# Kernel tuning notes

Measured on AMD Instinct MI355X. Metric: run time of the kernel, lower is better.

The kernel has to match this reference:

```python
import jax, jax.numpy as jnp
import numpy as np

B, C, H, W = 8, 256, 128, 128
INTER = 64      # in_channels // 4
C8 = INTER // 8 # query/key channels


def setup_inputs() -> dict:
    key = jax.random.key(0)
    ks = jax.random.split(key, 12)
    f = lambda k, shp, s=0.05: (jax.random.normal(k, shp, jnp.float32) * s)
    return dict(
        x_exmplar=f(ks[0], (B, C, H, W), 1.0),
        x_query=f(ks[1], (B, C, H, W), 1.0),
        conv_ex_w=f(ks[2], (INTER, C, 3, 3)),
        bn_ex_s=jnp.ones((INTER,), jnp.float32), bn_ex_b=jnp.zeros((INTER,), jnp.float32),
        conv_q_w=f(ks[3], (INTER, C, 3, 3)),
        bn_q_s=jnp.ones((INTER,), jnp.float32), bn_q_b=jnp.zeros((INTER,), jnp.float32),
        q_w=f(ks[4], (C8, INTER)), q_b=jnp.zeros((C8,), jnp.float32),
        k_w=f(ks[5], (C8, INTER)), k_b=jnp.zeros((C8,), jnp.float32),
        v_w=f(ks[6], (INTER, INTER)), v_b=jnp.zeros((INTER,), jnp.float32),
        gamma_1=jnp.float32(0.1), gamma_2=jnp.float32(0.1),
        tail_ex_w=f(ks[7], (C, INTER, 3, 3)),
        bn_tex_s=jnp.ones((C,), jnp.float32), bn_tex_b=jnp.zeros((C,), jnp.float32),
        tail_q_w=f(ks[8], (C, INTER, 3, 3)),
        bn_tq_s=jnp.ones((C,), jnp.float32), bn_tq_b=jnp.zeros((C,), jnp.float32),
    )


def _conv_bn_relu(x, w, s, b):
    # 3x3 conv (pad 1, no bias) + eval-mode BatchNorm (running mean 0 / var 1 at init) + ReLU
    y = jax.lax.conv_general_dilated(x, w, (1, 1), ((1, 1), (1, 1)),
                                     dimension_numbers=('NCHW', 'OIHW', 'NCHW'))
    return jax.nn.relu(y * s[None, :, None, None] + b[None, :, None, None])


def _rattention(xe, xq, qw, qb, kw, kb, vw, vb, g1, g2):
    b_, c_, h_, w_ = xq.shape
    q = jnp.einsum('oc,bchw->bohw', qw, xq) + qb[None, :, None, None]  # [B,C8,H,W]
    k = jnp.einsum('oc,bchw->bohw', kw, xe) + kb[None, :, None, None]
    v = jnp.einsum('oc,bchw->bohw', vw, xe) + vb[None, :, None, None]  # [B,INTER,H,W]
    # column (H-axis) energies, diagonal (self) masked with -inf
    eH = jnp.einsum('bciw,bcjw->biwj', q, k)                    # [B,H,W,H]
    diag = jnp.eye(h_, dtype=bool)[None, :, None, :]            # (1,H,1,H) over (i,j)
    eH = jnp.where(diag, -jnp.inf, eH)
    # row (W-axis) energies (no mask, matches original)
    eW = jnp.einsum('bchi,bchj->bhij', q, k)                    # [B,H,W,W]
    att = jax.nn.softmax(jnp.concatenate([eH, eW], axis=-1), axis=-1)
    attH, attW = att[..., :h_], att[..., h_:]
    outH = jnp.einsum('bcjw,bhwj->bchw', v, attH)
    outW = jnp.einsum('bchj,bhwj->bchw', v, attW)
    # LR diagonal branch; softmax over trailing singleton dim == ones (kept for fidelity)
    qd = jnp.diagonal(q, axis1=2, axis2=3)                      # [B,C8,H]
    kd = jnp.diagonal(k, axis1=2, axis2=3).transpose(0, 2, 1)   # [B,H,C8]
    vd = jnp.diagonal(v, axis1=2, axis2=3)                      # [B,INTER,H]
    eLR = jnp.einsum('bhc,bcj->bhj', kd, qd)                    # [B,H,H]
    outLR = jax.nn.softmax(jnp.einsum('bch,bhj->bcj', vd, eLR)[..., None], axis=3)  # [B,INTER,H,1]
    # RL branch: diagonal of the transposed map == same main diagonal -> identical to LR
    outRL = outLR
    s = outH + outW + outLR + outRL   # broadcast (B,INTER,H,1) over W
    return g1 * s + xe, g2 * s + xq


def reference(x_exmplar, x_query, conv_ex_w, bn_ex_s, bn_ex_b, conv_q_w, bn_q_s, bn_q_b,
              q_w, q_b, k_w, k_b, v_w, v_b, gamma_1, gamma_2,
              tail_ex_w, bn_tex_s, bn_tex_b, tail_q_w, bn_tq_s, bn_tq_b):
    xe = _conv_bn_relu(x_exmplar, conv_ex_w, bn_ex_s, bn_ex_b)
    xq = _conv_bn_relu(x_query, conv_q_w, bn_q_s, bn_q_b)
    for _ in range(2):  # recurrence=2
        xe, xq = _rattention(xe, xq, q_w, q_b, k_w, k_b, v_w, v_b, gamma_1, gamma_2)
    xe = _conv_bn_relu(xe, tail_ex_w, bn_tex_s, bn_tex_b)
    xq = _conv_bn_relu(xq, tail_q_w, bn_tq_s, bn_tq_b)
    return xe, xq
```

## Files before the change

### kernel.cpp

```cpp
#include <hip/hip_runtime.h>

constexpr int BB = 8;
constexpr int CC = 256;
constexpr int HH = 128;
constexpr int WW = 128;
constexpr int INTER = 64;
constexpr size_t NPIX = (size_t)HH * WW;
constexpr size_t C64SZ = (size_t)BB * INTER * NPIX;
constexpr size_t QSZ   = (size_t)BB * 8 * NPIX;
constexpr size_t STATSZ = (size_t)BB * HH * WW;
constexpr size_t OUTHALF = (size_t)BB * CC * NPIX;
constexpr size_t WT_ELEMS = (size_t)9 * 64 * 256;

typedef __attribute__((ext_vector_type(8))) __bf16 bf16x8;
typedef __attribute__((ext_vector_type(4))) float f32x4;
typedef __attribute__((ext_vector_type(4))) short short4v;

__device__ inline short f2bf(float f) {
    union { float f; unsigned u; } a; a.f = f;
    unsigned r = a.u + 0x7fffu + ((a.u >> 16) & 1u);
    return (short)(r >> 16);
}

__global__ __launch_bounds__(256) void wprep_kernel(
    const float* __restrict__ wgt, short* __restrict__ wt, int OC, int IC)
{
    int idx = blockIdx.x * 256 + threadIdx.x;
    int n = 9 * OC * IC;
    if (idx >= n) return;
    int ic = idx & (IC - 1);
    int t  = idx / IC;
    int oc = t & (OC - 1);
    int pos = t / OC;
    wt[idx] = f2bf(wgt[((size_t)oc * IC + ic) * 9 + pos]);
}

template<int IC, int OC, int R, int NT>
__global__ __launch_bounds__(256, 2) void conv_mfma(
    const float* __restrict__ x, const short* __restrict__ wt,
    const float* __restrict__ bns, const float* __restrict__ bnb,
    float* __restrict__ out)
{
    constexpr int ROWS = R + 2;
    constexpr int NCH  = IC / 32;
    constexpr int NPIXT = R * 128;
    constexpr int NWN  = NPIXT / (NT * 16);

    __shared__ __align__(16) short xs[ROWS * 130 * 40];

    const int tid = threadIdx.x;
    const int b   = blockIdx.x;
    const int h0  = blockIdx.y * R;
    const int l   = tid & 63;
    const int ln  = l & 15;
    const int q   = l >> 4;
    const int wv  = tid >> 6;
    const int nbase = (wv % NWN) * (NT * 16);
    const int oc0w  = (wv / NWN) * 64;

    f32x4 acc[4][NT];
#pragma unroll
    for (int mt = 0; mt < 4; ++mt)
#pragma unroll
        for (int nt = 0; nt < NT; ++nt)
            acc[mt][nt] = (f32x4){0.f, 0.f, 0.f, 0.f};

    const float* xb = x + (size_t)b * IC * NPIX;

    for (int ch = 0; ch < NCH; ++ch) {
        const int ic0 = ch * 32;
        constexpr int UNITS = ROWS * 8;
        for (int u = 0; u < UNITS; u += 2) {
            int unit = u + (tid >> 7);
            int col  = tid & 127;
            int row  = unit >> 3;
            int icg  = unit & 7;
            int ic   = ic0 + icg * 4;
            int grow = h0 - 1 + row;
            short4v pk;
            if ((unsigned)grow < 128u) {
                const float* p = xb + ((size_t)ic * 128 + grow) * 128 + col;
                pk.x = f2bf(p[0]);
                pk.y = f2bf(p[16384]);
                pk.z = f2bf(p[32768]);
                pk.w = f2bf(p[49152]);
            } else {
                pk.x = 0; pk.y = 0; pk.z = 0; pk.w = 0;
            }
            *(short4v*)&xs[(row * 130 + col + 1) * 40 + icg * 4] = pk;
        }
        if (tid < ROWS * 16) {
            int row  = tid >> 4;
            int colh = (tid & 8) ? 129 : 0;
            int icg  = tid & 7;
            short4v z; z.x = 0; z.y = 0; z.z = 0; z.w = 0;
            *(short4v*)&xs[(row * 130 + colh) * 40 + icg * 4] = z;
        }
        __syncthreads();

        for (int dh = 0; dh < 3; ++dh) {
#pragma unroll
            for (int dw = 0; dw < 3; ++dw) {
                const int pos = dh * 3 + dw;
                bf16x8 a[4];
#pragma unroll
                for (int mt = 0; mt < 4; ++mt)
                    a[mt] = *(const bf16x8*)(wt +
                        (size_t)(pos * OC + oc0w + mt * 16 + ln) * IC + ic0 + q * 8);
#pragma unroll
                for (int nt = 0; nt < NT; ++nt) {
                    int pix  = nbase + nt * 16 + ln;
                    int rowi = (pix >> 7) + dh;
                    int wpos = (pix & 127) + dw;
                    bf16x8 bfr = *(const bf16x8*)&xs[(rowi * 130 + wpos) * 40 + q * 8];
#pragma unroll
                    for (int mt = 0; mt < 4; ++mt)
                        acc[mt][nt] = __builtin_amdgcn_mfma_f32_16x16x32_bf16(
                            a[mt], bfr, acc[mt][nt], 0, 0, 0);
                }
            }
        }
        __syncthreads();
    }

#pragma unroll
    for (int mt = 0; mt < 4; ++mt) {
#pragma unroll
        for (int r = 0; r < 4; ++r) {
            int oc = oc0w + mt * 16 + q * 4 + r;
            float s   = bns[oc];
            float bb2 = bnb[oc];
#pragma unroll
            for (int nt = 0; nt < NT; ++nt) {
                int pix = nbase + nt * 16 + ln;
                int h = h0 + (pix >> 7), w = pix & 127;
                float v = fmaxf(acc[mt][nt][r] * s + bb2, 0.f);
                out[(((size_t)b * OC + oc) * 128 + h) * 128 + w] = v;
            }
        }
    }
}

__global__ __launch_bounds__(256) void qk_kernel(
    const float* __restrict__ xq, const float* __restrict__ xe,
    const float* __restrict__ qw, const float* __restrict__ qb,
    const float* __restrict__ kw, const float* __restrict__ kb,
    float* __restrict__ q, float* __restrict__ k)
{
    size_t p = (size_t)blockIdx.x * 256 + threadIdx.x;
    int b = (int)(p >> 14);
    int pix = (int)(p & 16383);
    const float* xqb = xq + (size_t)b * 64 * NPIX + pix;
    const float* xeb = xe + (size_t)b * 64 * NPIX + pix;
    float qa[8], ka[8];
#pragma unroll
    for (int o = 0; o < 8; ++o) { qa[o] = qb[o]; ka[o] = kb[o]; }
    for (int c = 0; c < 64; ++c) {
        float xv = xqb[(size_t)c * NPIX];
        float ev = xeb[(size_t)c * NPIX];
#pragma unroll
        for (int o = 0; o < 8; ++o) {
            qa[o] += qw[o * 64 + c] * xv;
            ka[o] += kw[o * 64 + c] * ev;
        }
    }
#pragma unroll
    for (int o = 0; o < 8; ++o) {
        q[((size_t)b * 8 + o) * NPIX + pix] = qa[o];
        k[((size_t)b * 8 + o) * NPIX + pix] = ka[o];
    }
}

__global__ __launch_bounds__(256) void v_kernel(
    const float* __restrict__ xe,
    const float* __restrict__ vw, const float* __restrict__ vb,
    float* __restrict__ v)
{
    size_t p = (size_t)blockIdx.x * 256 + threadIdx.x;
    int b = (int)(p >> 14);
    int pix = (int)(p & 16383);
    int oc0 = blockIdx.y * 32;
    const float* xeb = xe + (size_t)b * 64 * NPIX + pix;
    float acc[32];
#pragma unroll
    for (int o = 0; o < 32; ++o) acc[o] = vb[oc0 + o];
    for (int c = 0; c < 64; ++c) {
        float ev = xeb[(size_t)c * NPIX];
#pragma unroll
        for (int o = 0; o < 32; ++o) acc[o] += vw[(oc0 + o) * 64 + c] * ev;
    }
#pragma unroll
    for (int o = 0; o < 32; ++o)
        v[((size_t)b * 64 + oc0 + o) * NPIX + pix] = acc[o];
}

__global__ __launch_bounds__(256) void attn_col_kernel(
    const float* __restrict__ q, const float* __restrict__ k,
    const float* __restrict__ v,
    float* __restrict__ outT, float* __restrict__ mC, float* __restrict__ sC)
{
    __shared__ float qs[8][128];
    __shared__ float ks[8][128];
    __shared__ float vs[64][129];
    __shared__ float E[32][129];

    const int tid = threadIdx.x;
    const int w = blockIdx.x;
    const int b = blockIdx.y;

    for (int i = tid; i < 1024; i += 256) {
        int c = i >> 7, h = i & 127;
        qs[c][h] = q[(((size_t)b * 8 + c) * 128 + h) * 128 + w];
        ks[c][h] = k[(((size_t)b * 8 + c) * 128 + h) * 128 + w];
    }
    for (int i = tid; i < 8192; i += 256) {
        int c = i >> 7, j = i & 127;
        vs[c][j] = v[(((size_t)b * 64 + c) * 128 + j) * 128 + w];
    }
    __syncthreads();

    const int jj = tid & 127;
    const int hi = tid >> 7;

    for (int hc = 0; hc < 4; ++hc) {
        const int h0 = hc * 32;
#pragma unroll
        for (int e = 0; e < 16; ++e) {
            int i = e * 2 + hi;
            float a = 0.f;
#pragma unroll
            for (int c = 0; c < 8; ++c) a += qs[c][h0 + i] * ks[c][jj];
            if (h0 + i == jj) a = -1e30f;
            E[i][jj] = a;
        }
        __syncthreads();
        if (tid < 32) {
            int i = tid;
            float m = -1e30f;
            for (int j = 0; j < 128; ++j) m = fmaxf(m, E[i][j]);
            float s = 0.f;
            for (int j = 0; j < 128; ++j) {
                float pp = __expf(E[i][j] - m);
                E[i][j] = pp;
                s += pp;
            }
            mC[((size_t)b * 128 + (h0 + i)) * 128 + w] = m;
            sC[((size_t)b * 128 + (h0 + i)) * 128 + w] = s;
        }
        __syncthreads();
        {
            int c0 = (tid & 15) * 4;
            int i0 = (tid >> 4) * 2;
            float acc[4][2];
#pragma unroll
            for (int a = 0; a < 4; ++a) { acc[a][0] = 0.f; acc[a][1] = 0.f; }
            for (int j = 0; j < 128; ++j) {
                float p0 = E[i0][j], p1 = E[i0 + 1][j];
#pragma unroll
                for (int a = 0; a < 4; ++a) {
                    float vv = vs[c0 + a][j];
                    acc[a][0] += vv * p0;
                    acc[a][1] += vv * p1;
                }
            }
#pragma unroll
            for (int a = 0; a < 4; ++a) {
                size_t base = (((size_t)b * 128 + w) * 64 + (c0 + a)) * 128 + h0 + i0;
                outT[base]     = acc[a][0];
                outT[base + 1] = acc[a][1];
            }
        }
        __syncthreads();
    }
}

__global__ __launch_bounds__(256) void attn_row_kernel(
    const float* __restrict__ q, const float* __restrict__ k,
    const float* __restrict__ v,
    float* __restrict__ outS, float* __restrict__ mR, float* __restrict__ sR)
{
    __shared__ float qs[8][128];
    __shared__ float ks[8][128];
    __shared__ float vs[64][129];
    __shared__ float E[32][129];

    const int tid = threadIdx.x;
    const int h = blockIdx.x;
    const int b = blockIdx.y;

    for (int i = tid; i < 1024; i += 256) {
        int c = i >> 7, x = i & 127;
        qs[c][x] = q[(((size_t)b * 8 + c) * 128 + h) * 128 + x];
        ks[c][x] = k[(((size_t)b * 8 + c) * 128 + h) * 128 + x];
    }
    for (int i = tid; i < 8192; i += 256) {
        int c = i >> 7, j = i & 127;
        vs[c][j] = v[(((size_t)b * 64 + c) * 128 + h) * 128 + j];
    }
    __syncthreads();

    const int jj = tid & 127;
    const int hi = tid >> 7;

    for (int wc = 0; wc < 4; ++wc) {
        const int w0 = wc * 32;
#pragma unroll
        for (int e = 0; e < 16; ++e) {
            int i = e * 2 + hi;
            float a = 0.f;
#pragma unroll
            for (int c = 0; c < 8; ++c) a += qs[c][w0 + i] * ks[c][jj];
            E[i][jj] = a;
        }
        __syncthreads();
        if (tid < 32) {
            int i = tid;
            float m = -1e30f;
            for (int j = 0; j < 128; ++j) m = fmaxf(m, E[i][j]);
            float s = 0.f;
            for (int j = 0; j < 128; ++j) {
                float pp = __expf(E[i][j] - m);
                E[i][j] = pp;
                s += pp;
            }
            mR[((size_t)b * 128 + h) * 128 + (w0 + i)] = m;
            sR[((size_t)b * 128 + h) * 128 + (w0 + i)] = s;
        }
        __syncthreads();
        {
            int c0 = (tid & 15) * 4;
            int i0 = (tid >> 4) * 2;
            float acc[4][2];
#pragma unroll
            for (int a = 0; a < 4; ++a) { acc[a][0] = 0.f; acc[a][1] = 0.f; }
            for (int j = 0; j < 128; ++j) {
                float p0 = E[i0][j], p1 = E[i0 + 1][j];
#pragma unroll
                for (int a = 0; a < 4; ++a) {
                    float vv = vs[c0 + a][j];
                    acc[a][0] += vv * p0;
                    acc[a][1] += vv * p1;
                }
            }
#pragma unroll
            for (int a = 0; a < 4; ++a) {
                size_t base = (((size_t)b * 64 + (c0 + a)) * 128 + h) * 128 + w0 + i0;
                outS[base]     = acc[a][0];
                outS[base + 1] = acc[a][1];
            }
        }
        __syncthreads();
    }
}

__global__ __launch_bounds__(256) void merge_kernel(
    const float* __restrict__ T1, const float* __restrict__ S2,
    const float* __restrict__ mC, const float* __restrict__ sC,
    const float* __restrict__ mR, const float* __restrict__ sR,
    const float* __restrict__ g1p, const float* __restrict__ g2p,
    float* __restrict__ xe, float* __restrict__ xq)
{
    __shared__ float mc[128], sc[128], mr[128], sr[128];
    const int tid = threadIdx.x;
    const int h = blockIdx.x;
    const int b = blockIdx.y;
    if (tid < 128) {
        size_t o = ((size_t)b * 128 + h) * 128 + tid;
        mc[tid] = mC[o]; sc[tid] = sC[o];
        mr[tid] = mR[o]; sr[tid] = sR[o];
    }
    float g1 = g1p[0], g2 = g2p[0];
    __syncthreads();
    for (int i = tid; i < 8192; i += 256) {
        int c = i >> 7, w = i & 127;
        float oc_ = T1[(((size_t)b * 128 + w) * 64 + c) * 128 + h];
        float ow_ = S2[(((size_t)b * 64 + c) * 128 + h) * 128 + w];
        float m  = fmaxf(mc[w], mr[w]);
        float ec = __expf(mc[w] - m);
        float er = __expf(mr[w] - m);
        float denom = sc[w] * ec + sr[w] * er;
        float sval = (oc_ * ec + ow_ * er) / denom + 2.0f;
        size_t p = (((size_t)b * 64 + c) * 128 + h) * 128 + w;
        xe[p] += g1 * sval;
        xq[p] += g2 * sval;
    }
}

extern "C" void kernel_launch(void* const* d_in, const int* in_sizes, int n_in,
                              void* d_out, int out_size, void* d_ws, size_t ws_size,
                              hipStream_t stream)
{
    const float* x_ex = (const float*)d_in[0];
    const float* x_q  = (const float*)d_in[1];
    const float* cew  = (const float*)d_in[2];
    const float* bes  = (const float*)d_in[3];
    const float* beb  = (const float*)d_in[4];
    const float* cqw  = (const float*)d_in[5];
    const float* bqs  = (const float*)d_in[6];
    const float* bqb  = (const float*)d_in[7];
    const float* qw   = (const float*)d_in[8];
    const float* qb   = (const float*)d_in[9];
    const float* kw   = (const float*)d_in[10];
    const float* kb   = (const float*)d_in[11];
    const float* vw   = (const float*)d_in[12];
    const float* vb   = (const float*)d_in[13];
    const float* g1   = (const float*)d_in[14];
    const float* g2   = (const float*)d_in[15];
    const float* tew  = (const float*)d_in[16];
    const float* bts  = (const float*)d_in[17];
    const float* btb  = (const float*)d_in[18];
    const float* tqw  = (const float*)d_in[19];
    const float* btqs = (const float*)d_in[20];
    const float* btqb = (const float*)d_in[21];

    float* out = (float*)d_out;

    short* wt0 = (short*)d_ws;
    short* wt1 = wt0 + WT_ELEMS;
    short* wt2 = wt1 + WT_ELEMS;
    short* wt3 = wt2 + WT_ELEMS;
    float* Wf  = (float*)(wt3 + WT_ELEMS);
    float* xe = Wf;
    float* xq = Wf + C64SZ;
    float* v  = Wf + 2 * C64SZ;
    float* q  = Wf + 3 * C64SZ;
    float* k  = q + QSZ;

    float* T1 = out;
    float* S2 = out + C64SZ;
    float* mC = out + 2 * C64SZ;
    float* sC = mC + STATSZ;
    float* mR = sC + STATSZ;
    float* sR = mR + STATSZ;

    wprep_kernel<<<576, 256, 0, stream>>>(cew, wt0, 64, 256);
    wprep_kernel<<<576, 256, 0, stream>>>(cqw, wt1, 64, 256);
    wprep_kernel<<<576, 256, 0, stream>>>(tew, wt2, 256, 64);
    wprep_kernel<<<576, 256, 0, stream>>>(tqw, wt3, 256, 64);

    conv_mfma<256, 64, 2, 4><<<dim3(8, 64), 256, 0, stream>>>(x_ex, wt0, bes, beb, xe);
    conv_mfma<256, 64, 2, 4><<<dim3(8, 64), 256, 0, stream>>>(x_q,  wt1, bqs, bqb, xq);

    for (int round = 0; round < 2; ++round) {
        qk_kernel<<<512, 256, 0, stream>>>(xq, xe, qw, qb, kw, kb, q, k);
        v_kernel<<<dim3(512, 2), 256, 0, stream>>>(xe, vw, vb, v);
        attn_col_kernel<<<dim3(128, 8), 256, 0, stream>>>(q, k, v, T1, mC, sC);
        attn_row_kernel<<<dim3(128, 8), 256, 0, stream>>>(q, k, v, S2, mR, sR);
        merge_kernel<<<dim3(128, 8), 256, 0, stream>>>(T1, S2, mC, sC, mR, sR, g1, g2, xe, xq);
    }

    conv_mfma<64, 256, 1, 8><<<dim3(8, 128), 256, 0, stream>>>(xe, wt2, bts, btb, out);
    conv_mfma<64, 256, 1, 8><<<dim3(8, 128), 256, 0, stream>>>(xq, wt3, btqs, btqb, out + OUTHALF);
}
```

Before: 1.567 ms.

## Prefetch conv input tiles in registers, widen head conv blocks, parallelize softmax

The conv kernel now loads the next 32-channel input chunk into registers with vectorized float4 loads while MFMAs run on the current chunk, then converts and writes it to LDS after a barrier. This is meant to hide global load latency that was previously fully exposed. The head conv moves to 512-thread blocks with fewer N tiles per wave. In both attention kernels the row softmax is spread across all 256 threads with shuffle reductions instead of 32 serial threads. The register prefetch buffer raises register pressure, which may limit occupancy.

Measured after the change: 1.597 ms. About the same (+1.9%).

```diff
diff --git a/kernel.cpp b/kernel.cpp
--- a/kernel.cpp
+++ b/kernel.cpp
@@ -35,8 +35,8 @@
     wt[idx] = f2bf(wgt[((size_t)oc * IC + ic) * 9 + pos]);
 }
 
-template<int IC, int OC, int R, int NT>
-__global__ __launch_bounds__(256, 2) void conv_mfma(
+template<int IC, int OC, int R, int NT, int BLK, int MINW>
+__global__ __launch_bounds__(BLK, MINW) void conv_mfma(
     const float* __restrict__ x, const short* __restrict__ wt,
     const float* __restrict__ bns, const float* __restrict__ bnb,
     float* __restrict__ out)
@@ -45,6 +45,8 @@
     constexpr int NCH  = IC / 32;
     constexpr int NPIXT = R * 128;
     constexpr int NWN  = NPIXT / (NT * 16);
+    constexpr int TOTAL_UNITS = ROWS * 8 * 32;
+    constexpr int NU   = TOTAL_UNITS / BLK;
 
     __shared__ __align__(16) short xs[ROWS * 130 * 40];
 
@@ -67,37 +69,65 @@
 
     const float* xb = x + (size_t)b * IC * NPIX;
 
+    f32x4 pf[NU][4];
+
+    if (tid < ROWS * 16) {
+        int row  = tid >> 4;
+        int colh = (tid & 8) ? 129 : 0;
+        int icg  = tid & 7;
+        short4v z; z.x = 0; z.y = 0; z.z = 0; z.w = 0;
+        *(short4v*)&xs[(row * 130 + colh) * 40 + icg * 4] = z;
+    }
+
+    auto issue = [&](int ch) {
+        const int ic0 = ch * 32;
+#pragma unroll
+        for (int i = 0; i < NU; ++i) {
+            int u    = i * BLK + tid;
+            int row  = u >> 8;
+            int icq  = (u >> 5) & 7;
+            int colq = u & 31;
+            int grow = h0 - 1 + row;
+            if ((unsigned)grow < 128u) {
+                const float* p = xb + ((size_t)(ic0 + icq * 4) * 128 + grow) * 128 + colq * 4;
+#pragma unroll
+                for (int j = 0; j < 4; ++j)
+                    pf[i][j] = *(const f32x4*)(p + (size_t)j * NPIX);
+            } else {
+#pragma unroll
+                for (int j = 0; j < 4; ++j)
+                    pf[i][j] = (f32x4){0.f, 0.f, 0.f, 0.f};
+            }
+        }
+    };
+
+    auto commit = [&]() {
+#pragma unroll
+        for (int i = 0; i < NU; ++i) {
+            int u    = i * BLK + tid;
+            int row  = u >> 8;
+            int icq  = (u >> 5) & 7;
+            int colq = u & 31;
+#pragma unroll
+            for (int k = 0; k < 4; ++k) {
+                short4v pk;
+                pk.x = f2bf(pf[i][0][k]);
+                pk.y = f2bf(pf[i][1][k]);
+                pk.z = f2bf(pf[i][2][k]);
+                pk.w = f2bf(pf[i][3][k]);
+                *(short4v*)&xs[(row * 130 + colq * 4 + k + 1) * 40 + icq * 4] = pk;
+            }
+        }
+    };
+
+    issue(0);
+    commit();
+    __syncthreads();
+
     for (int ch = 0; ch < NCH; ++ch) {
+        if (ch + 1 < NCH) issue(ch + 1);
+
         const int ic0 = ch * 32;
-        constexpr int UNITS = ROWS * 8;
-        for (int u = 0; u < UNITS; u += 2) {
-            int unit = u + (tid >> 7);
-            int col  = tid & 127;
-            int row  = unit >> 3;
-            int icg  = unit & 7;
-            int ic   = ic0 + icg * 4;
-            int grow = h0 - 1 + row;
-            short4v pk;
-            if ((unsigned)grow < 128u) {
-                const float* p = xb + ((size_t)ic * 128 + grow) * 128 + col;
-                pk.x = f2bf(p[0]);
-                pk.y = f2bf(p[16384]);
-                pk.z = f2bf(p[32768]);
-                pk.w = f2bf(p[49152]);
-            } else {
-                pk.x = 0; pk.y = 0; pk.z = 0; pk.w = 0;
-            }
-            *(short4v*)&xs[(row * 130 + col + 1) * 40 + icg * 4] = pk;
-        }
-        if (tid < ROWS * 16) {
-            int row  = tid >> 4;
-            int colh = (tid & 8) ? 129 : 0;
-            int icg  = tid & 7;
-            short4v z; z.x = 0; z.y = 0; z.z = 0; z.w = 0;
-            *(short4v*)&xs[(row * 130 + colh) * 40 + icg * 4] = z;
-        }
-        __syncthreads();
-
         for (int dh = 0; dh < 3; ++dh) {
 #pragma unroll
             for (int dw = 0; dw < 3; ++dw) {
@@ -121,6 +151,10 @@
             }
         }
         __syncthreads();
+        if (ch + 1 < NCH) {
+            commit();
+            __syncthreads();
+        }
     }
 
 #pragma unroll
@@ -234,18 +268,29 @@
             E[i][jj] = a;
         }
         __syncthreads();
-        if (tid < 32) {
-            int i = tid;
+        {
+            int row = tid >> 3, l8 = tid & 7;
             float m = -1e30f;
-            for (int j = 0; j < 128; ++j) m = fmaxf(m, E[i][j]);
+#pragma unroll
+            for (int t = 0; t < 16; ++t) m = fmaxf(m, E[row][l8 + t * 8]);
+            m = fmaxf(m, __shfl_xor(m, 1));
+            m = fmaxf(m, __shfl_xor(m, 2));
+            m = fmaxf(m, __shfl_xor(m, 4));
             float s = 0.f;
-            for (int j = 0; j < 128; ++j) {
-                float pp = __expf(E[i][j] - m);
-                E[i][j] = pp;
+#pragma unroll
+            for (int t = 0; t < 16; ++t) {
+                int j = l8 + t * 8;
+                float pp = __expf(E[row][j] - m);
+                E[row][j] = pp;
                 s += pp;
             }
-            mC[((size_t)b * 128 + (h0 + i)) * 128 + w] = m;
-            sC[((size_t)b * 128 + (h0 + i)) * 128 + w] = s;
+            s += __shfl_xor(s, 1);
+            s += __shfl_xor(s, 2);
+            s += __shfl_xor(s, 4);
+            if (l8 == 0) {
+                mC[((size_t)b * 128 + (h0 + row)) * 128 + w] = m;
+                sC[((size_t)b * 128 + (h0 + row)) * 128 + w] = s;
+            }
         }
         __syncthreads();
         {
@@ -313,18 +358,29 @@
             E[i][jj] = a;
         }
         __syncthreads();
-        if (tid < 32) {
-            int i = tid;
+        {
+            int row = tid >> 3, l8 = tid & 7;
             float m = -1e30f;
-            for (int j = 0; j < 128; ++j) m = fmaxf(m, E[i][j]);
+#pragma unroll
+            for (int t = 0; t < 16; ++t) m = fmaxf(m, E[row][l8 + t * 8]);
+            m = fmaxf(m, __shfl_xor(m, 1));
+            m = fmaxf(m, __shfl_xor(m, 2));
+            m = fmaxf(m, __shfl_xor(m, 4));
             float s = 0.f;
-            for (int j = 0; j < 128; ++j) {
-                float pp = __expf(E[i][j] - m);
-                E[i][j] = pp;
+#pragma unroll
+            for (int t = 0; t < 16; ++t) {
+                int j = l8 + t * 8;
+                float pp = __expf(E[row][j] - m);
+                E[row][j] = pp;
                 s += pp;
             }
-            mR[((size_t)b * 128 + h) * 128 + (w0 + i)] = m;
-            sR[((size_t)b * 128 + h) * 128 + (w0 + i)] = s;
+            s += __shfl_xor(s, 1);
+            s += __shfl_xor(s, 2);
+            s += __shfl_xor(s, 4);
+            if (l8 == 0) {
+                mR[((size_t)b * 128 + h) * 128 + (w0 + row)] = m;
+                sR[((size_t)b * 128 + h) * 128 + (w0 + row)] = s;
+            }
         }
         __syncthreads();
         {
@@ -438,8 +494,8 @@
     wprep_kernel<<<576, 256, 0, stream>>>(tew, wt2, 256, 64);
     wprep_kernel<<<576, 256, 0, stream>>>(tqw, wt3, 256, 64);
 
-    conv_mfma<256, 64, 2, 4><<<dim3(8, 64), 256, 0, stream>>>(x_ex, wt0, bes, beb, xe);
-    conv_mfma<256, 64, 2, 4><<<dim3(8, 64), 256, 0, stream>>>(x_q,  wt1, bqs, bqb, xq);
+    conv_mfma<256, 64, 2, 2, 512, 4><<<dim3(8, 64), 512, 0, stream>>>(x_ex, wt0, bes, beb, xe);
+    conv_mfma<256, 64, 2, 2, 512, 4><<<dim3(8, 64), 512, 0, stream>>>(x_q,  wt1, bqs, bqb, xq);
 
     for (int round = 0; round < 2; ++round) {
         qk_kernel<<<512, 256, 0, stream>>>(xq, xe, qw, qb, kw, kb, q, k);
@@ -449,6 +505,6 @@
         merge_kernel<<<dim3(128, 8), 256, 0, stream>>>(T1, S2, mC, sC, mR, sR, g1, g2, xe, xq);
     }
 
-    conv_mfma<64, 256, 1, 8><<<dim3(8, 128), 256, 0, stream>>>(xe, wt2, bts, btb, out);
-    conv_mfma<64, 256, 1, 8><<<dim3(8, 128), 256, 0, stream>>>(xq, wt3, btqs, btqb, out + OUTHALF);
-}
+    conv_mfma<64, 256, 1, 8, 256, 2><<<dim3(8, 128), 256, 0, stream>>>(xe, wt2, bts, btb, out);
+    conv_mfma<64, 256, 1, 8, 256, 2><<<dim3(8, 128), 256, 0, stream>>>(xq, wt3, btqs, btqb, out + OUTHALF);
+}
```
